# Kernel tuning notes

Measured on AMD Instinct MI355X. Metric: run time of the kernel, lower is better.

Reference implementation:

```python
import jax, jax.numpy as jnp
import numpy as np

EMBED_DIM = 768
NUM_HEADS = 12
HEAD_DIM = EMBED_DIM // NUM_HEADS
HIDDEN_DIM = int(EMBED_DIM * 4.0)
LN_EPS = 1e-5


def setup_inputs() -> dict:
    key = jax.random.key(0)
    ks = jax.random.split(key, 8)
    B, N, C = 16, 1024, EMBED_DIM
    s = 0.02
    return {
        "x": jax.random.normal(ks[0], (B, N, C), dtype=jnp.float32),
        "ln1_g": jnp.ones((C,), jnp.float32),
        "ln1_b": jnp.zeros((C,), jnp.float32),
        "qkv_w": jax.random.normal(ks[1], (C, 3 * C), jnp.float32) * s,
        "qkv_b": jnp.zeros((3 * C,), jnp.float32),
        "proj_w": jax.random.normal(ks[2], (C, C), jnp.float32) * s,
        "proj_b": jnp.zeros((C,), jnp.float32),
        "ln2_g": jnp.ones((C,), jnp.float32),
        "ln2_b": jnp.zeros((C,), jnp.float32),
        "fc1_w": jax.random.normal(ks[3], (C, HIDDEN_DIM), jnp.float32) * s,
        "fc1_b": jnp.zeros((HIDDEN_DIM,), jnp.float32),
        "fc2_w": jax.random.normal(ks[4], (HIDDEN_DIM, C), jnp.float32) * s,
        "fc2_b": jnp.zeros((C,), jnp.float32),
    }


def _layernorm(x, g, b):
    mu = jnp.mean(x, axis=-1, keepdims=True)
    var = jnp.mean(jnp.square(x - mu), axis=-1, keepdims=True)
    return (x - mu) * jax.lax.rsqrt(var + LN_EPS) * g + b


def _attention(x, qkv_w, qkv_b, proj_w, proj_b):
    B, N, C = x.shape
    qkv = x @ qkv_w + qkv_b                       # [B,N,3C]
    qkv = qkv.reshape(B, N, 3, NUM_HEADS, HEAD_DIM)
    q, k, v = qkv[:, :, 0], qkv[:, :, 1], qkv[:, :, 2]  # [B,N,H,D]
    scale = HEAD_DIM ** -0.5
    attn = jnp.einsum("bqhd,bkhd->bhqk", q, k) * scale
    attn = jax.nn.softmax(attn, axis=-1)
    out = jnp.einsum("bhqk,bkhd->bqhd", attn, v).reshape(B, N, C)
    return out @ proj_w + proj_b


def reference(x, ln1_g, ln1_b, qkv_w, qkv_b, proj_w, proj_b,
              ln2_g, ln2_b, fc1_w, fc1_b, fc2_w, fc2_b):
    x = x + _attention(_layernorm(x, ln1_g, ln1_b), qkv_w, qkv_b, proj_w, proj_b)
    h = _layernorm(x, ln2_g, ln2_b)
    h = jax.nn.gelu(h @ fc1_w + fc1_b, approximate=False)
    return x + (h @ fc2_w + fc2_b)
```

## Files before the change

### kernel.cpp

```cpp
#include <hip/hip_runtime.h>
#include <math.h>

#define SEQ 1024
#define NH 12
#define CC 768

using short8 = __attribute__((ext_vector_type(8))) short;
using bf16x8 = __attribute__((ext_vector_type(8))) __bf16;
using f32x4  = __attribute__((ext_vector_type(4))) float;

__device__ __forceinline__ unsigned short f2bf(float f){
  unsigned u = __builtin_bit_cast(unsigned, f);
  u += 0x7FFF + ((u >> 16) & 1);
  return (unsigned short)(u >> 16);
}

__device__ __forceinline__ void gload16(const void* g, void* l){
  __builtin_amdgcn_global_load_lds((const __attribute__((address_space(1))) unsigned int*)g,
                                   (__attribute__((address_space(3))) unsigned int*)l, 16, 0, 0);
}
__device__ __forceinline__ bf16x8 lds_frag(const unsigned short* p){
  return __builtin_bit_cast(bf16x8, *(const short8*)p);
}
__device__ __forceinline__ bf16x8 gld_frag(const unsigned short* p){
  return __builtin_bit_cast(bf16x8, *(const short8*)p);
}

__global__ __launch_bounds__(256) void wtrans(const float* __restrict__ W,
                                              unsigned short* __restrict__ Wt,
                                              int K, int N){
  __shared__ float tile[32][33];
  int tx = threadIdx.x & 31, ty = threadIdx.x >> 5;
  int n0 = blockIdx.x * 32, k0 = blockIdx.y * 32;
#pragma unroll
  for (int j = 0; j < 4; j++)
    tile[ty + j*8][tx] = W[(size_t)(k0 + ty + j*8) * N + n0 + tx];
  __syncthreads();
#pragma unroll
  for (int j = 0; j < 4; j++)
    Wt[(size_t)(n0 + ty + j*8) * K + k0 + tx] = f2bf(tile[tx][ty + j*8]);
}

__global__ __launch_bounds__(64) void ln_k(const float* __restrict__ x,
                                           const float* __restrict__ g,
                                           const float* __restrict__ be,
                                           unsigned short* __restrict__ out){
  const int row = blockIdx.x;
  const int lane = threadIdx.x;
  const float* xr = x + (size_t)row * CC;
  float4 v[3];
  float s = 0.f, sq = 0.f;
#pragma unroll
  for (int j = 0; j < 3; j++){
    v[j] = *(const float4*)(xr + lane*4 + j*256);
    s  += v[j].x + v[j].y + v[j].z + v[j].w;
    sq += v[j].x*v[j].x + v[j].y*v[j].y + v[j].z*v[j].z + v[j].w*v[j].w;
  }
#pragma unroll
  for (int d = 1; d < 64; d <<= 1){ s += __shfl_xor(s, d); sq += __shfl_xor(sq, d); }
  float mu = s * (1.0f/CC);
  float var = sq * (1.0f/CC) - mu*mu;
  float rstd = rsqrtf(var + 1e-5f);
  unsigned short* orow = out + (size_t)row * CC;
#pragma unroll
  for (int j = 0; j < 3; j++){
    int cb = lane*4 + j*256;
    float4 gv = *(const float4*)(g + cb);
    float4 bv = *(const float4*)(be + cb);
    ushort4 o;
    o.x = f2bf((v[j].x - mu)*rstd*gv.x + bv.x);
    o.y = f2bf((v[j].y - mu)*rstd*gv.y + bv.y);
    o.z = f2bf((v[j].z - mu)*rstd*gv.z + bv.z);
    o.w = f2bf((v[j].w - mu)*rstd*gv.w + bv.w);
    *(ushort4*)(orow + cb) = o;
  }
}

__global__ __launch_bounds__(256) void vextract(const unsigned short* __restrict__ qkv,
                                                unsigned short* __restrict__ vT){
  __shared__ unsigned short tile[32][33];
  int bh = blockIdx.y;
  int b = bh / NH, h = bh % NH;
  int tt = blockIdx.x & 31, dt = blockIdx.x >> 5;
  int tx = threadIdx.x & 31, ty = threadIdx.x >> 5;
#pragma unroll
  for (int j = 0; j < 4; j++)
    tile[ty + j*8][tx] = qkv[(size_t)(b*SEQ + tt*32 + ty + j*8)*2304 + 1536 + h*64 + dt*32 + tx];
  __syncthreads();
#pragma unroll
  for (int j = 0; j < 4; j++)
    vT[((size_t)bh*64 + dt*32 + ty + j*8)*SEQ + tt*32 + tx] = tile[tx][ty + j*8];
}

template<int MODE>
__global__ __launch_bounds__(512, 2) void gemm256(const unsigned short* __restrict__ A,
                                                  const unsigned short* __restrict__ Bt,
                                                  const float* __restrict__ bias,
                                                  const float* __restrict__ resid,
                                                  void* __restrict__ outp,
                                                  int M, int N, int K){
  __shared__ __align__(16) unsigned short lds[2][4][128*64];
  const int t = threadIdx.x;
  const int lane = t & 63, w = t >> 6;
  const int wr = w >> 2, wc = w & 3;
  const int l15 = lane & 15, lg = lane >> 4;
  const int ntn = N >> 8;
  const int bid = blockIdx.x;
  const int bm = bid / ntn, bn = bid % ntn;

  const unsigned short* gA0 = A  + (size_t)bm*256*K;
  const unsigned short* gA1 = gA0 + (size_t)128*K;
  const unsigned short* gB0 = Bt + (size_t)bn*256*K;
  const unsigned short* gB1 = gB0 + (size_t)128*K;

  const int csw = (t & 7) ^ ((t >> 3) & 7);
  const size_t off0 = (size_t)(t >> 3)*K + csw*8;
  const size_t off1 = off0 + (size_t)64*K;

  auto stageh = [&](int bi, int rg, const unsigned short* gb, int kt){
    const unsigned short* s = gb + (size_t)kt*64;
    unsigned short* d = &lds[bi][rg][0];
    gload16(s + off0, d + t*8);
    gload16(s + off1, d + 4096 + t*8);
  };

  const int cx0 = (lg ^ (l15 & 7)) * 8;
  const int cx1 = ((4 + lg) ^ (l15 & 7)) * 8;
  const int rB = (wc & 1)*64 + l15;

  f32x4 acc[8][4] = {};
  const int nk = K >> 6;

  stageh(0,0,gA0,0); stageh(0,1,gA1,0); stageh(0,2,gB0,0); stageh(0,3,gB1,0);
  stageh(1,0,gA0,1); stageh(1,1,gA1,1); stageh(1,2,gB0,1);
  asm volatile("s_waitcnt vmcnt(6)" ::: "memory");
  __builtin_amdgcn_sched_barrier(0);
  __builtin_amdgcn_s_barrier();

  bf16x8 alo[4][2], ahi[4][2], bfl[2][2], bfh[2][2];
  for (int kt = 0; kt < nk; ++kt){
    const int buf = kt & 1;
    const unsigned short* pA = &lds[buf][wr][0];
    const unsigned short* pB = &lds[buf][2 + (wc >> 1)][0];

#pragma unroll
    for (int m = 0; m < 4; m++){
      alo[m][0] = lds_frag(pA + (m*16 + l15)*64 + cx0);
      alo[m][1] = lds_frag(pA + (m*16 + l15)*64 + cx1);
    }
#pragma unroll
    for (int n = 0; n < 2; n++){
      bfl[n][0] = lds_frag(pB + (rB + n*16)*64 + cx0);
      bfl[n][1] = lds_frag(pB + (rB + n*16)*64 + cx1);
    }
    if (kt + 1 < nk) stageh((kt+1)&1, 3, gB1, kt+1);
    __builtin_amdgcn_sched_barrier(0);
    __builtin_amdgcn_s_barrier();
    asm volatile("s_waitcnt lgkmcnt(0)" ::: "memory");
    __builtin_amdgcn_sched_barrier(0);
    __builtin_amdgcn_s_setprio(1);
#pragma unroll
    for (int m = 0; m < 4; m++)
#pragma unroll
      for (int n = 0; n < 2; n++){
        acc[m][n] = __builtin_amdgcn_mfma_f32_16x16x32_bf16(alo[m][0], bfl[n][0], acc[m][n], 0,0,0);
        acc[m][n] = __builtin_amdgcn_mfma_f32_16x16x32_bf16(alo[m][1], bfl[n][1], acc[m][n], 0,0,0);
      }
    __builtin_amdgcn_s_setprio(0);
    __builtin_amdgcn_sched_barrier(0);
    __builtin_amdgcn_s_barrier();

#pragma unroll
    for (int m = 0; m < 4; m++){
      ahi[m][0] = lds_frag(pA + ((m+4)*16 + l15)*64 + cx0);
      ahi[m][1] = lds_frag(pA + ((m+4)*16 + l15)*64 + cx1);
    }
    if (kt + 2 < nk) stageh(buf, 0, gA0, kt+2);
    __builtin_amdgcn_sched_barrier(0);
    __builtin_amdgcn_s_barrier();
    asm volatile("s_waitcnt lgkmcnt(0)" ::: "memory");
    __builtin_amdgcn_sched_barrier(0);
    __builtin_amdgcn_s_setprio(1);
#pragma unroll
    for (int m = 0; m < 4; m++)
#pragma unroll
      for (int n = 0; n < 2; n++){
        acc[m+4][n] = __builtin_amdgcn_mfma_f32_16x16x32_bf16(ahi[m][0], bfl[n][0], acc[m+4][n], 0,0,0);
        acc[m+4][n] = __builtin_amdgcn_mfma_f32_16x16x32_bf16(ahi[m][1], bfl[n][1], acc[m+4][n], 0,0,0);
      }
    __builtin_amdgcn_s_setprio(0);
    __builtin_amdgcn_sched_barrier(0);
    __builtin_amdgcn_s_barrier();

#pragma unroll
    for (int n = 0; n < 2; n++){
      bfh[n][0] = lds_frag(pB + (rB + (n+2)*16)*64 + cx0);
      bfh[n][1] = lds_frag(pB + (rB + (n+2)*16)*64 + cx1);
    }
    if (kt + 2 < nk) stageh(buf, 1, gA1, kt+2);
    __builtin_amdgcn_sched_barrier(0);
    __builtin_amdgcn_s_barrier();
    asm volatile("s_waitcnt lgkmcnt(0)" ::: "memory");
    __builtin_amdgcn_sched_barrier(0);
    __builtin_amdgcn_s_setprio(1);
#pragma unroll
    for (int m = 0; m < 4; m++)
#pragma unroll
      for (int n = 0; n < 2; n++){
        acc[m+4][n+2] = __builtin_amdgcn_mfma_f32_16x16x32_bf16(ahi[m][0], bfh[n][0], acc[m+4][n+2], 0,0,0);
        acc[m+4][n+2] = __builtin_amdgcn_mfma_f32_16x16x32_bf16(ahi[m][1], bfh[n][1], acc[m+4][n+2], 0,0,0);
      }
    __builtin_amdgcn_s_setprio(0);
    __builtin_amdgcn_sched_barrier(0);
    __builtin_amdgcn_s_barrier();

    if (kt + 2 < nk) stageh(buf, 2, gB0, kt+2);
    __builtin_amdgcn_sched_barrier(0);
    __builtin_amdgcn_s_barrier();
    __builtin_amdgcn_s_setprio(1);
#pragma unroll
    for (int m = 0; m < 4; m++)
#pragma unroll
      for (int n = 0; n < 2; n++){
        acc[m][n+2] = __builtin_amdgcn_mfma_f32_16x16x32_bf16(alo[m][0], bfh[n][0], acc[m][n+2], 0,0,0);
        acc[m][n+2] = __builtin_amdgcn_mfma_f32_16x16x32_bf16(alo[m][1], bfh[n][1], acc[m][n+2], 0,0,0);
      }
    __builtin_amdgcn_s_setprio(0);
    if (kt < nk - 1){
      if (kt + 2 < nk) { asm volatile("s_waitcnt vmcnt(6)" ::: "memory"); }
      else             { asm volatile("s_waitcnt vmcnt(0)" ::: "memory"); }
    }
    __builtin_amdgcn_sched_barrier(0);
    __builtin_amdgcn_s_barrier();
  }

  const int row0 = bm*256 + wr*128 + lg*4;
  const int col0 = bn*256 + wc*64;
  if constexpr (MODE == 1){
#pragma unroll
    for (int n = 0; n < 4; n++){
      int c = col0 + n*16 + l15;
      float bv = bias[c];
#pragma unroll
      for (int m = 0; m < 8; m++){
        int r = row0 + m*16;
#pragma unroll
        for (int i = 0; i < 4; i++){
          size_t idx = (size_t)(r + i) * N + c;
          ((float*)outp)[idx] = resid[idx] + acc[m][n][i] + bv;
        }
      }
    }
  } else {
#pragma unroll
    for (int n = 0; n < 4; n++){
      float bv = bias[col0 + n*16 + l15];
#pragma unroll
      for (int m = 0; m < 8; m++)
#pragma unroll
        for (int i = 0; i < 4; i++){
          float v = acc[m][n][i] + bv;
          if constexpr (MODE == 2){
            float u = v + 0.044715f*v*v*v;
            float a = fminf(-1.5957691216057308f*u, 80.f);
            float e = __expf(a);
            v = 0.5f*v*(1.0f + (1.f - e)/(1.f + e));
          }
          acc[m][n][i] = v;
        }
    }
    unsigned int* O = (unsigned int*)outp;
    const int src0 = lg*16 + ((2*l15) & 15);
    const int src1 = lg*16 + ((2*l15 + 1) & 15);
    const bool sel = (l15 < 8);
#pragma unroll
    for (int p = 0; p < 2; p++)
#pragma unroll
      for (int m = 0; m < 8; m++)
#pragma unroll
        for (int i = 0; i < 4; i++){
          float e0a = __shfl(acc[m][2*p][i],   src0);
          float e0b = __shfl(acc[m][2*p+1][i], src0);
          float e1a = __shfl(acc[m][2*p][i],   src1);
          float e1b = __shfl(acc[m][2*p+1][i], src1);
          float v0 = sel ? e0a : e0b;
          float v1 = sel ? e1a : e1b;
          unsigned int pk = (unsigned int)f2bf(v0) | ((unsigned int)f2bf(v1) << 16);
          int r = row0 + m*16 + i;
          int cu = (col0 + p*32)/2 + l15;
          O[(size_t)r * (N >> 1) + cu] = pk;
        }
  }
}

__global__ __launch_bounds__(256, 2) void attn_k(const unsigned short* __restrict__ qkv,
                                                 const unsigned short* __restrict__ vT,
                                                 unsigned short* __restrict__ aout){
  __shared__ __align__(16) unsigned short Ks[2][64*64];
  __shared__ __align__(16) unsigned short Vs[2][64*64];
  __shared__ __align__(16) unsigned short Ps[4][32*64];
  const int t = threadIdx.x, lane = t & 63, w = t >> 6;
  const int l15 = lane & 15, lg = lane >> 4;
  const int qt = blockIdx.x;
  const int bh = blockIdx.y;
  const int b = bh / NH, h = bh % NH;
  const size_t qrow0 = (size_t)b * SEQ + qt*128 + w*32;

  bf16x8 qf[2][2];
#pragma unroll
  for (int nf = 0; nf < 2; nf++)
#pragma unroll
    for (int ks = 0; ks < 2; ks++)
      qf[nf][ks] = gld_frag(qkv + (qrow0 + nf*16 + l15)*2304 + h*64 + ks*32 + lg*8);

  f32x4 o[2][4] = {};
  float mold[2] = {-3.0e38f, -3.0e38f};
  float lsum[2] = {0.f, 0.f};

  const unsigned short* Kgl = qkv + (size_t)b * SEQ * 2304 + 768 + h*64;
  const unsigned short* Vgl = vT + (size_t)bh * 64 * SEQ;

  auto stageKV = [&](int bufi, int kt){
#pragma unroll
    for (int i = 0; i < 2; i++){
      int idx = i*256 + t; int r = idx >> 3; int s = idx & 7; int ss = s ^ (r & 7);
      gload16(Kgl + (size_t)(kt*64 + r)*2304 + ss*8, &Ks[bufi][idx*8]);
    }
#pragma unroll
    for (int i = 0; i < 2; i++){
      int idx = i*256 + t; int r = idx >> 3; int s = idx & 7; int ss = s ^ (r & 7);
      gload16(Vgl + (size_t)r*SEQ + kt*64 + ss*8, &Vs[bufi][idx*8]);
    }
  };

  stageKV(0, 0);
  __syncthreads();
  int buf = 0;

  for (int kt = 0; kt < 16; ++kt){
    if (kt + 1 < 16) stageKV(buf ^ 1, kt + 1);

    f32x4 st[4][2] = {};
#pragma unroll
    for (int ks = 0; ks < 2; ks++){
      bf16x8 kf[4];
#pragma unroll
      for (int mf = 0; mf < 4; mf++){
        int rr = mf*16 + l15;
        int sc = (ks*4 + lg) ^ (rr & 7);
        kf[mf] = lds_frag(&Ks[buf][rr*64 + sc*8]);
      }
#pragma unroll
      for (int mf = 0; mf < 4; mf++)
#pragma unroll
        for (int nf = 0; nf < 2; nf++)
          st[mf][nf] = __builtin_amdgcn_mfma_f32_16x16x32_bf16(kf[mf], qf[nf][ks], st[mf][nf], 0, 0, 0);
    }

    float fsc[2];
#pragma unroll
    for (int nf = 0; nf < 2; nf++){
      float mx = -3.0e38f;
#pragma unroll
      for (int mf = 0; mf < 4; mf++)
#pragma unroll
        for (int i = 0; i < 4; i++){
          float sv = st[mf][nf][i] * 0.125f;
          st[mf][nf][i] = sv;
          mx = fmaxf(mx, sv);
        }
      mx = fmaxf(mx, __shfl_xor(mx, 16));
      mx = fmaxf(mx, __shfl_xor(mx, 32));
      float nm = fmaxf(mold[nf], mx);
      float f = __expf(mold[nf] - nm);
      mold[nf] = nm;
      float rs = 0.f;
#pragma unroll
      for (int mf = 0; mf < 4; mf++)
#pragma unroll
        for (int i = 0; i < 4; i++){
          float p = __expf(st[mf][nf][i] - nm);
          st[mf][nf][i] = p;
          rs += p;
        }
      rs += __shfl_xor(rs, 16);
      rs += __shfl_xor(rs, 32);
      lsum[nf] = lsum[nf]*f + rs;
      fsc[nf] = f;
    }

#pragma unroll
    for (int nf = 0; nf < 2; nf++)
#pragma unroll
      for (int mf = 0; mf < 4; mf++)
#pragma unroll
        for (int i = 0; i < 4; i++){
          int rP = nf*16 + l15;
          int col = mf*16 + lg*4 + i;
          Ps[w][rP*64 + (col ^ ((rP & 7) << 3))] = f2bf(st[mf][nf][i]);
        }

#pragma unroll
    for (int mm = 0; mm < 2; mm++)
#pragma unroll
      for (int i = 0; i < 4; i++){
        float fo = __shfl(fsc[mm], lg*4 + i);
#pragma unroll
        for (int df = 0; df < 4; df++)
          o[mm][df][i] *= fo;
      }

#pragma unroll
    for (int ks = 0; ks < 2; ks++){
      bf16x8 pf[2], vf[4];
#pragma unroll
      for (int mm = 0; mm < 2; mm++){
        int rP = mm*16 + l15;
        int sc = (ks*4 + lg) ^ (rP & 7);
        pf[mm] = lds_frag(&Ps[w][rP*64 + sc*8]);
      }
#pragma unroll
      for (int df = 0; df < 4; df++){
        int rr = df*16 + l15;
        int sc = (ks*4 + lg) ^ (rr & 7);
        vf[df] = lds_frag(&Vs[buf][rr*64 + sc*8]);
      }
#pragma unroll
      for (int mm = 0; mm < 2; mm++)
#pragma unroll
        for (int df = 0; df < 4; df++)
          o[mm][df] = __builtin_amdgcn_mfma_f32_16x16x32_bf16(pf[mm], vf[df], o[mm][df], 0, 0, 0);
    }
    __syncthreads();
    buf ^= 1;
  }

#pragma unroll
  for (int mm = 0; mm < 2; mm++){
    float li = 1.0f / lsum[mm];
#pragma unroll
    for (int i = 0; i < 4; i++){
      float rl = __shfl(li, lg*4 + i);
      size_t r = qrow0 + mm*16 + lg*4 + i;
#pragma unroll
      for (int df = 0; df < 4; df++)
        aout[r*CC + h*64 + df*16 + l15] = f2bf(o[mm][df][i] * rl);
    }
  }
}

extern "C" void kernel_launch(void* const* d_in, const int* in_sizes, int n_in,
                              void* d_out, int out_size, void* d_ws, size_t ws_size,
                              hipStream_t stream){
  (void)in_sizes; (void)n_in; (void)out_size; (void)ws_size;
  const float* x      = (const float*)d_in[0];
  const float* ln1_g  = (const float*)d_in[1];
  const float* ln1_b  = (const float*)d_in[2];
  const float* qkv_w  = (const float*)d_in[3];
  const float* qkv_b  = (const float*)d_in[4];
  const float* proj_w = (const float*)d_in[5];
  const float* proj_b = (const float*)d_in[6];
  const float* ln2_g  = (const float*)d_in[7];
  const float* ln2_b  = (const float*)d_in[8];
  const float* fc1_w  = (const float*)d_in[9];
  const float* fc1_b  = (const float*)d_in[10];
  const float* fc2_w  = (const float*)d_in[11];
  const float* fc2_b  = (const float*)d_in[12];
  float* out = (float*)d_out;
  char* ws = (char*)d_ws;

  unsigned short* ln_out  = (unsigned short*)(ws);
  unsigned short* qkv_buf = (unsigned short*)(ws + 25165824);
  unsigned short* vTb     = (unsigned short*)(ws + 100663296);
  unsigned short* attn    = (unsigned short*)(ws + 125829120);
  unsigned short* hbuf    = qkv_buf;
  char* wbase = ws + 150994944;
  unsigned short* wq = (unsigned short*)(wbase);
  unsigned short* wp = (unsigned short*)(wbase + 3538944);
  unsigned short* w1 = (unsigned short*)(wbase + 4718592);
  unsigned short* w2 = (unsigned short*)(wbase + 9437184);

  wtrans<<<dim3(72, 24), 256, 0, stream>>>(qkv_w, wq, 768, 2304);
  wtrans<<<dim3(24, 24), 256, 0, stream>>>(proj_w, wp, 768, 768);
  wtrans<<<dim3(96, 24), 256, 0, stream>>>(fc1_w, w1, 768, 3072);
  wtrans<<<dim3(24, 96), 256, 0, stream>>>(fc2_w, w2, 3072, 768);

  ln_k<<<16384, 64, 0, stream>>>(x, ln1_g, ln1_b, ln_out);
  gemm256<0><<<64*9, 512, 0, stream>>>(ln_out, wq, qkv_b, nullptr, qkv_buf, 16384, 2304, 768);
  vextract<<<dim3(64, 192), 256, 0, stream>>>(qkv_buf, vTb);
  attn_k<<<dim3(8, 192), 256, 0, stream>>>(qkv_buf, vTb, attn);
  gemm256<1><<<64*3, 512, 0, stream>>>(attn, wp, proj_b, x, out, 16384, 768, 768);
  ln_k<<<16384, 64, 0, stream>>>(out, ln2_g, ln2_b, ln_out);
  gemm256<2><<<64*12, 512, 0, stream>>>(ln_out, w1, fc1_b, nullptr, hbuf, 16384, 3072, 768);
  gemm256<1><<<64*3, 512, 0, stream>>>(hbuf, w2, fc2_b, out, out, 16384, 768, 3072);
}
```

Before: 662.0 us.

## Restructure GEMM main loop to simple double-buffer with split-K fragment pipelining

Replaces the quarter-tile staggered prefetch schedule, which used many block barriers per K step, with a plain double buffer. Each iteration issues all global-to-LDS loads for the next K tile up front and splits the MFMA work by K-half, so LDS fragment reads for the next phase overlap with current MFMAs via partial lgkmcnt waits. Each warp now reads all four B column fragments per K half, and the loop uses a single barrier per iteration. Prefetch depth drops from two tiles to one, and the loop ends with a full vmcnt(0) wait, which may expose global load latency.

```diff
diff --git a/kernel.cpp b/kernel.cpp
--- a/kernel.cpp
+++ b/kernel.cpp
@@ -99,7 +99,8 @@
                                                   const float* __restrict__ resid,
                                                   void* __restrict__ outp,
                                                   int M, int N, int K){
-  __shared__ __align__(16) unsigned short lds[2][4][128*64];
+  __shared__ __align__(16) unsigned short Ab[2][256*64];
+  __shared__ __align__(16) unsigned short Bb[2][256*64];
   const int t = threadIdx.x;
   const int lane = t & 63, w = t >> 6;
   const int wr = w >> 2, wc = w & 3;
@@ -108,128 +109,99 @@
   const int bid = blockIdx.x;
   const int bm = bid / ntn, bn = bid % ntn;
 
-  const unsigned short* gA0 = A  + (size_t)bm*256*K;
-  const unsigned short* gA1 = gA0 + (size_t)128*K;
-  const unsigned short* gB0 = Bt + (size_t)bn*256*K;
-  const unsigned short* gB1 = gB0 + (size_t)128*K;
+  const unsigned short* gA = A  + (size_t)bm*256*K;
+  const unsigned short* gB = Bt + (size_t)bn*256*K;
 
   const int csw = (t & 7) ^ ((t >> 3) & 7);
-  const size_t off0 = (size_t)(t >> 3)*K + csw*8;
-  const size_t off1 = off0 + (size_t)64*K;
-
-  auto stageh = [&](int bi, int rg, const unsigned short* gb, int kt){
-    const unsigned short* s = gb + (size_t)kt*64;
-    unsigned short* d = &lds[bi][rg][0];
-    gload16(s + off0, d + t*8);
-    gload16(s + off1, d + 4096 + t*8);
+  const int trow = t >> 3;
+
+  auto stage4 = [&](unsigned short* dst, const unsigned short* gb, int kt){
+    const unsigned short* s = gb + (size_t)kt*64 + csw*8;
+#pragma unroll
+    for (int q = 0; q < 4; q++)
+      gload16(s + (size_t)(q*64 + trow)*K, dst + (q*512 + t)*8);
   };
 
   const int cx0 = (lg ^ (l15 & 7)) * 8;
   const int cx1 = ((4 + lg) ^ (l15 & 7)) * 8;
-  const int rB = (wc & 1)*64 + l15;
 
   f32x4 acc[8][4] = {};
   const int nk = K >> 6;
 
-  stageh(0,0,gA0,0); stageh(0,1,gA1,0); stageh(0,2,gB0,0); stageh(0,3,gB1,0);
-  stageh(1,0,gA0,1); stageh(1,1,gA1,1); stageh(1,2,gB0,1);
-  asm volatile("s_waitcnt vmcnt(6)" ::: "memory");
+  stage4(Ab[0], gA, 0);
+  stage4(Bb[0], gB, 0);
+  asm volatile("s_waitcnt vmcnt(0)" ::: "memory");
   __builtin_amdgcn_sched_barrier(0);
   __builtin_amdgcn_s_barrier();
 
-  bf16x8 alo[4][2], ahi[4][2], bfl[2][2], bfh[2][2];
   for (int kt = 0; kt < nk; ++kt){
     const int buf = kt & 1;
-    const unsigned short* pA = &lds[buf][wr][0];
-    const unsigned short* pB = &lds[buf][2 + (wc >> 1)][0];
-
-#pragma unroll
-    for (int m = 0; m < 4; m++){
-      alo[m][0] = lds_frag(pA + (m*16 + l15)*64 + cx0);
-      alo[m][1] = lds_frag(pA + (m*16 + l15)*64 + cx1);
-    }
-#pragma unroll
-    for (int n = 0; n < 2; n++){
-      bfl[n][0] = lds_frag(pB + (rB + n*16)*64 + cx0);
-      bfl[n][1] = lds_frag(pB + (rB + n*16)*64 + cx1);
-    }
-    if (kt + 1 < nk) stageh((kt+1)&1, 3, gB1, kt+1);
-    __builtin_amdgcn_sched_barrier(0);
-    __builtin_amdgcn_s_barrier();
+    const unsigned short* pA = Ab[buf] + wr*128*64;
+    const unsigned short* pB = Bb[buf];
+    bf16x8 aL0[4], aH0[4], aL1[4], aH1[4], b0[4], b1[4];
+
+#pragma unroll
+    for (int m = 0; m < 4; m++) aL0[m] = lds_frag(pA + (m*16 + l15)*64 + cx0);
+#pragma unroll
+    for (int n = 0; n < 4; n++) b0[n]  = lds_frag(pB + (wc*64 + n*16 + l15)*64 + cx0);
+    __builtin_amdgcn_sched_barrier(0);
+    if (kt + 1 < nk){
+      stage4(Ab[buf^1], gA, kt+1);
+      stage4(Bb[buf^1], gB, kt+1);
+    }
+    __builtin_amdgcn_sched_barrier(0);
+#pragma unroll
+    for (int m = 0; m < 4; m++) aH0[m] = lds_frag(pA + ((m+4)*16 + l15)*64 + cx0);
+    __builtin_amdgcn_sched_barrier(0);
+    asm volatile("s_waitcnt lgkmcnt(4)" ::: "memory");
+    __builtin_amdgcn_sched_barrier(0);
+    __builtin_amdgcn_s_setprio(1);
+#pragma unroll
+    for (int m = 0; m < 4; m++)
+#pragma unroll
+      for (int n = 0; n < 4; n++)
+        acc[m][n] = __builtin_amdgcn_mfma_f32_16x16x32_bf16(aL0[m], b0[n], acc[m][n], 0,0,0);
+    __builtin_amdgcn_s_setprio(0);
+    __builtin_amdgcn_sched_barrier(0);
+#pragma unroll
+    for (int m = 0; m < 4; m++) aL1[m] = lds_frag(pA + (m*16 + l15)*64 + cx1);
+#pragma unroll
+    for (int n = 0; n < 4; n++) b1[n]  = lds_frag(pB + (wc*64 + n*16 + l15)*64 + cx1);
+    __builtin_amdgcn_sched_barrier(0);
+    asm volatile("s_waitcnt lgkmcnt(8)" ::: "memory");
+    __builtin_amdgcn_sched_barrier(0);
+    __builtin_amdgcn_s_setprio(1);
+#pragma unroll
+    for (int m = 0; m < 4; m++)
+#pragma unroll
+      for (int n = 0; n < 4; n++)
+        acc[m+4][n] = __builtin_amdgcn_mfma_f32_16x16x32_bf16(aH0[m], b0[n], acc[m+4][n], 0,0,0);
+    __builtin_amdgcn_s_setprio(0);
+    __builtin_amdgcn_sched_barrier(0);
+#pragma unroll
+    for (int m = 0; m < 4; m++) aH1[m] = lds_frag(pA + ((m+4)*16 + l15)*64 + cx1);
+    __builtin_amdgcn_sched_barrier(0);
+    asm volatile("s_waitcnt lgkmcnt(4)" ::: "memory");
+    __builtin_amdgcn_sched_barrier(0);
+    __builtin_amdgcn_s_setprio(1);
+#pragma unroll
+    for (int m = 0; m < 4; m++)
+#pragma unroll
+      for (int n = 0; n < 4; n++)
+        acc[m][n] = __builtin_amdgcn_mfma_f32_16x16x32_bf16(aL1[m], b1[n], acc[m][n], 0,0,0);
+    __builtin_amdgcn_s_setprio(0);
+    __builtin_amdgcn_sched_barrier(0);
     asm volatile("s_waitcnt lgkmcnt(0)" ::: "memory");
     __builtin_amdgcn_sched_barrier(0);
     __builtin_amdgcn_s_setprio(1);
 #pragma unroll
     for (int m = 0; m < 4; m++)
 #pragma unroll
-      for (int n = 0; n < 2; n++){
-        acc[m][n] = __builtin_amdgcn_mfma_f32_16x16x32_bf16(alo[m][0], bfl[n][0], acc[m][n], 0,0,0);
-        acc[m][n] = __builtin_amdgcn_mfma_f32_16x16x32_bf16(alo[m][1], bfl[n][1], acc[m][n], 0,0,0);
-      }
+      for (int n = 0; n < 4; n++)
+        acc[m+4][n] = __builtin_amdgcn_mfma_f32_16x16x32_bf16(aH1[m], b1[n], acc[m+4][n], 0,0,0);
     __builtin_amdgcn_s_setprio(0);
     __builtin_amdgcn_sched_barrier(0);
-    __builtin_amdgcn_s_barrier();
-
-#pragma unroll
-    for (int m = 0; m < 4; m++){
-      ahi[m][0] = lds_frag(pA + ((m+4)*16 + l15)*64 + cx0);
-      ahi[m][1] = lds_frag(pA + ((m+4)*16 + l15)*64 + cx1);
-    }
-    if (kt + 2 < nk) stageh(buf, 0, gA0, kt+2);
-    __builtin_amdgcn_sched_barrier(0);
-    __builtin_amdgcn_s_barrier();
-    asm volatile("s_waitcnt lgkmcnt(0)" ::: "memory");
-    __builtin_amdgcn_sched_barrier(0);
-    __builtin_amdgcn_s_setprio(1);
-#pragma unroll
-    for (int m = 0; m < 4; m++)
-#pragma unroll
-      for (int n = 0; n < 2; n++){
-        acc[m+4][n] = __builtin_amdgcn_mfma_f32_16x16x32_bf16(ahi[m][0], bfl[n][0], acc[m+4][n], 0,0,0);
-        acc[m+4][n] = __builtin_amdgcn_mfma_f32_16x16x32_bf16(ahi[m][1], bfl[n][1], acc[m+4][n], 0,0,0);
-      }
-    __builtin_amdgcn_s_setprio(0);
-    __builtin_amdgcn_sched_barrier(0);
-    __builtin_amdgcn_s_barrier();
-
-#pragma unroll
-    for (int n = 0; n < 2; n++){
-      bfh[n][0] = lds_frag(pB + (rB + (n+2)*16)*64 + cx0);
-      bfh[n][1] = lds_frag(pB + (rB + (n+2)*16)*64 + cx1);
-    }
-    if (kt + 2 < nk) stageh(buf, 1, gA1, kt+2);
-    __builtin_amdgcn_sched_barrier(0);
-    __builtin_amdgcn_s_barrier();
-    asm volatile("s_waitcnt lgkmcnt(0)" ::: "memory");
-    __builtin_amdgcn_sched_barrier(0);
-    __builtin_amdgcn_s_setprio(1);
-#pragma unroll
-    for (int m = 0; m < 4; m++)
-#pragma unroll
-      for (int n = 0; n < 2; n++){
-        acc[m+4][n+2] = __builtin_amdgcn_mfma_f32_16x16x32_bf16(ahi[m][0], bfh[n][0], acc[m+4][n+2], 0,0,0);
-        acc[m+4][n+2] = __builtin_amdgcn_mfma_f32_16x16x32_bf16(ahi[m][1], bfh[n][1], acc[m+4][n+2], 0,0,0);
-      }
-    __builtin_amdgcn_s_setprio(0);
-    __builtin_amdgcn_sched_barrier(0);
-    __builtin_amdgcn_s_barrier();
-
-    if (kt + 2 < nk) stageh(buf, 2, gB0, kt+2);
-    __builtin_amdgcn_sched_barrier(0);
-    __builtin_amdgcn_s_barrier();
-    __builtin_amdgcn_s_setprio(1);
-#pragma unroll
-    for (int m = 0; m < 4; m++)
-#pragma unroll
-      for (int n = 0; n < 2; n++){
-        acc[m][n+2] = __builtin_amdgcn_mfma_f32_16x16x32_bf16(alo[m][0], bfh[n][0], acc[m][n+2], 0,0,0);
-        acc[m][n+2] = __builtin_amdgcn_mfma_f32_16x16x32_bf16(alo[m][1], bfh[n][1], acc[m][n+2], 0,0,0);
-      }
-    __builtin_amdgcn_s_setprio(0);
-    if (kt < nk - 1){
-      if (kt + 2 < nk) { asm volatile("s_waitcnt vmcnt(6)" ::: "memory"); }
-      else             { asm volatile("s_waitcnt vmcnt(0)" ::: "memory"); }
-    }
+    asm volatile("s_waitcnt vmcnt(0)" ::: "memory");
     __builtin_amdgcn_sched_barrier(0);
     __builtin_amdgcn_s_barrier();
   }
```

Result: slower. 683.7 us (+3.3%).
